# Kernel tuning notes

Measured on AMD Instinct MI355X. Metric: run time of the kernel, lower is better.

The kernel has to match this reference:

```python
import jax, jax.numpy as jnp
import numpy as np

D = 128          # embed_dim
NB = 30          # hardcoded neighbor count in neighbor_encoder
STEPS = 4        # process_steps
NSYM = 200000    # num_symbols (pad idx = NSYM)
B = 4096         # query batch
FEW = 5          # support pairs


def setup_inputs() -> dict:
    key = jax.random.key(0)
    ks = jax.random.split(key, 32)
    g = lambda i, shape, s=0.02: jax.random.normal(ks[i], shape, dtype=jnp.float32) * s
    inp = {}
    # embedding tables (row NSYM is padding, zeros)
    inp['emb'] = g(0, (NSYM + 1, D), 0.1).at[NSYM].set(0.0)
    inp['emb_var'] = g(1, (NSYM + 1, D), 0.1).at[NSYM].set(0.0)
    # neighbor attention (mean path)
    inp['nW'], inp['nWb'] = g(2, (D, 2 * D)), jnp.zeros((D,), jnp.float32)
    inp['nu'], inp['nub'] = g(3, (1, D)), jnp.zeros((1,), jnp.float32)
    # neighbor attention (var path)
    inp['nvW'], inp['nvWb'] = g(4, (D, 2 * D)), jnp.zeros((D,), jnp.float32)
    inp['nvu'], inp['nvub'] = g(5, (1, D)), jnp.zeros((1,), jnp.float32)
    # SupportEncoder: d_model=2D, d_inner=4D
    inp['p1W'], inp['p1b'] = g(6, (4 * D, 2 * D)), jnp.zeros((4 * D,), jnp.float32)
    inp['p2W'], inp['p2b'] = g(7, (2 * D, 4 * D)), jnp.zeros((2 * D,), jnp.float32)
    inp['ln_a'], inp['ln_b'] = jnp.ones((2 * D,), jnp.float32), jnp.zeros((2 * D,), jnp.float32)
    # QueryEncoder LSTMCell: input 2D, hidden 4D (torch gate order i,f,g,o)
    inp['Wih'], inp['Whh'] = g(8, (16 * D, 2 * D)), g(9, (16 * D, 4 * D))
    inp['bih'], inp['bhh'] = jnp.zeros((16 * D,), jnp.float32), jnp.zeros((16 * D,), jnp.float32)
    # connections: (..., 0)=relation idx, (..., 1)=entity idx
    inp['q_left'] = jax.random.randint(ks[10], (B, NB, 2), 0, NSYM, dtype=jnp.int32)
    inp['q_right'] = jax.random.randint(ks[11], (B, NB, 2), 0, NSYM, dtype=jnp.int32)
    inp['s_left'] = jax.random.randint(ks[12], (FEW, NB, 2), 0, NSYM, dtype=jnp.int32)
    inp['s_right'] = jax.random.randint(ks[13], (FEW, NB, 2), 0, NSYM, dtype=jnp.int32)
    return inp


def _layer_norm(z, a, b, eps=0.001):
    # faithful to torch: std with Bessel correction (ddof=1)
    mu = jnp.mean(z, axis=-1, keepdims=True)
    sigma = jnp.std(z, axis=-1, keepdims=True, ddof=1)
    return (z - mu) / (sigma + eps) * a + b


def reference(emb, emb_var, nW, nWb, nu, nub, nvW, nvWb, nvu, nvub,
              p1W, p1b, p2W, p2b, ln_a, ln_b, Wih, Whh, bih, bhh,
              q_left, q_right, s_left, s_right):

    def neighbor_encoder(conn):
        rel, ent = conn[..., 0], conn[..., 1]
        rel_e, ent_e = emb[rel], emb[ent]                      # [N, NB, D]
        cat = jnp.concatenate([rel_e, ent_e], axis=-1)         # [N, NB, 2D]
        a = jnp.tanh(cat @ nW.T + nWb) @ nu.T + nub            # [N, NB, 1]
        att = jax.nn.softmax(a[..., 0], axis=1)                # softmax over neighbors
        out = jnp.einsum('nk,nkd->nd', att, ent_e)
        rel_v, ent_v = emb_var[rel], emb_var[ent]
        catv = jnp.concatenate([rel_v, ent_v], axis=-1)
        av = jnp.tanh(catv @ nvW.T + nvWb) @ nvu.T + nvub
        attv = jax.nn.softmax(av[..., 0], axis=1)
        out_v = jnp.einsum('nk,nkd->nd', attv, ent_e)          # torch quirk: pools ent_embeds
        return jnp.tanh(out), jnp.tanh(out_v)

    def support_encoder(x):
        h = jax.nn.relu(x @ p1W.T + p1b) @ p2W.T + p2b
        return _layer_norm(h + x, ln_a, ln_b)

    def lstm_cell(x, h, c):
        gates = x @ Wih.T + bih + h @ Whh.T + bhh
        i, f, g_, o = jnp.split(gates, 4, axis=-1)
        c = jax.nn.sigmoid(f) * c + jax.nn.sigmoid(i) * jnp.tanh(g_)
        return jax.nn.sigmoid(o) * jnp.tanh(c), c

    def query_encoder(support, query):
        n = query.shape[0]
        h_r = jnp.zeros((n, 4 * D), query.dtype)
        c = jnp.zeros((n, 4 * D), query.dtype)
        h = query
        for _ in range(STEPS):
            h_r_, c = lstm_cell(query, h_r, c)
            h = query + h_r_[:, :2 * D]
            attn = jax.nn.softmax(h @ support.T, axis=1)
            r = attn @ support
            h_r = jnp.concatenate([h, r], axis=1)
        return h

    ql, qlv = neighbor_encoder(q_left)
    qr, qrv = neighbor_encoder(q_right)
    sl, slv = neighbor_encoder(s_left)
    sr, srv = neighbor_encoder(s_right)

    query = jnp.concatenate([ql, qr], axis=-1)       # [B, 2D]
    query_v = jnp.concatenate([qlv, qrv], axis=-1)
    support = jnp.concatenate([sl, sr], axis=-1)     # [FEW, 2D]
    support_v = jnp.concatenate([slv, srv], axis=-1)

    def match(q, s):
        s_g = support_encoder(s)
        q_g = support_encoder(q)
        q_f = query_encoder(s_g, q_g)
        s_mean = jnp.mean(s_g, axis=0, keepdims=True)  # [1, 2D]
        return (q_f @ s_mean.T)[:, 0]                  # [B]

    score = match(query, support)
    score_var = match(query_v, support_v)
    return jnp.stack([score, score_var])               # [2, B]
```

## Files before the change

kernel.cpp:

```cpp
#include <hip/hip_runtime.h>
#include <math.h>

#define DD    128
#define TWOD  256
#define FOURD 512
#define NBN   30
#define BQ    4096
#define FEWN  5
#define NSYM  200000
#define KTOT  768
#define NGATE 1024
#define ULIVE 256
#define TOTU  (2 * BQ + 2 * FEWN)
#define UPB   4
#define PSTR  136

typedef short bf16x8 __attribute__((ext_vector_type(8)));
typedef float f32x4 __attribute__((ext_vector_type(4)));

__device__ __forceinline__ float sigmoidf_(float x) { return 1.0f / (1.0f + expf(-x)); }

__device__ __forceinline__ float ftanh(float x) {
    float e = __expf(2.0f * x);
    return 1.0f - 2.0f / (e + 1.0f);
}

__device__ __forceinline__ unsigned short f2bf(float f) {
    unsigned int u = __float_as_uint(f);
    unsigned int r = (u + 0x7fffu + ((u >> 16) & 1u)) >> 16;
    return (unsigned short)r;
}

__device__ __forceinline__ float bf2f(unsigned short s) {
    return __uint_as_float(((unsigned int)s) << 16);
}

__device__ __forceinline__ bf16x8 pack8(float4 a, float4 b) {
    union { bf16x8 v; unsigned int u[4]; } r;
    r.u[0] = ((__float_as_uint(a.x) + 0x8000u) >> 16) | ((__float_as_uint(a.y) + 0x8000u) & 0xffff0000u);
    r.u[1] = ((__float_as_uint(a.z) + 0x8000u) >> 16) | ((__float_as_uint(a.w) + 0x8000u) & 0xffff0000u);
    r.u[2] = ((__float_as_uint(b.x) + 0x8000u) >> 16) | ((__float_as_uint(b.y) + 0x8000u) & 0xffff0000u);
    r.u[3] = ((__float_as_uint(b.z) + 0x8000u) >> 16) | ((__float_as_uint(b.w) + 0x8000u) & 0xffff0000u);
    return r.v;
}

__device__ __forceinline__ void gload_lds16(const void* g, void* l) {
    __builtin_amdgcn_global_load_lds((const __attribute__((address_space(1))) unsigned int*)g,
                                     (__attribute__((address_space(3))) unsigned int*)l,
                                     16, 0, 0);
}

__global__ __launch_bounds__(256) void k_prep(
    const float* __restrict__ Wih, const float* __restrict__ Whh,
    const float* __restrict__ bih, const float* __restrict__ bhh,
    const float* __restrict__ p1W, const float* __restrict__ p2W,
    const float* __restrict__ nW, const float* __restrict__ nvW,
    unsigned short* __restrict__ Wbf, float* __restrict__ biasR,
    float* __restrict__ p1WT, float* __restrict__ p2WT,
    unsigned short* __restrict__ Nbf)
{
    int idx = blockIdx.x * 256 + threadIdx.x;
    int stride = gridDim.x * 256;
    for (int i = idx; i < NGATE * KTOT; i += stride) {
        int n = i / KTOT, k = i - n * KTOT;
        int blk = n >> 6, rem = n & 63;
        int g = rem >> 4, ul = rem & 15;
        int u = blk * 16 + ul;
        int srcrow = g * 512 + u;
        float v = (k < TWOD) ? Wih[srcrow * TWOD + k] : Whh[srcrow * FOURD + (k - TWOD)];
        Wbf[i] = f2bf(v);
    }
    for (int n = idx; n < NGATE; n += stride) {
        int blk = n >> 6, rem = n & 63;
        int g = rem >> 4, ul = rem & 15;
        int u = blk * 16 + ul;
        int srcrow = g * 512 + u;
        biasR[n] = bih[srcrow] + bhh[srcrow];
    }
    for (int i = idx; i < FOURD * TWOD; i += stride) {
        int o = i / TWOD, j = i % TWOD;
        p1WT[j * FOURD + o] = p1W[o * TWOD + j];
    }
    for (int i = idx; i < TWOD * FOURD; i += stride) {
        int o = i / FOURD, j = i % FOURD;
        p2WT[j * TWOD + o] = p2W[o * FOURD + j];
    }
    for (int i = idx; i < 2 * DD * TWOD; i += stride) {
        float v = (i < DD * TWOD) ? nW[i] : nvW[i - DD * TWOD];
        Nbf[i] = f2bf(v);
    }
}

__global__ __launch_bounds__(256, 2) void k_neighbor_v4(
    const float* __restrict__ emb, const float* __restrict__ emb_var,
    const unsigned short* __restrict__ Nbf,
    const float* __restrict__ nWb, const float* __restrict__ nu,
    const float* __restrict__ nvWb, const float* __restrict__ nvu,
    const int* __restrict__ q_left, const int* __restrict__ q_right,
    const int* __restrict__ s_left, const int* __restrict__ s_right,
    float* __restrict__ query, float* __restrict__ support)
{
    const int tid  = threadIdx.x;
    const int wave = tid >> 6, lane = tid & 63;
    const int quad = lane >> 4, m15 = lane & 15;
    const int pw   = wave >> 1;
    const int wn   = wave & 1;
    const int u0   = blockIdx.x * UPB;

    __shared__ __align__(16) unsigned short Sg[4 * 32 * PSTR];
    __shared__ int   sidxL[UPB][64];
    __shared__ float aP[2][2][32];
    __shared__ float attL[2][32];

    {
        int un = tid >> 6, i = tid & 63;
        int uu_ = u0 + un; if (uu_ >= TOTU) uu_ = TOTU - 1;
        const int* conn;
        if (uu_ < BQ)                 conn = q_left  + uu_ * (NBN * 2);
        else if (uu_ < 2 * BQ)        conn = q_right + (uu_ - BQ) * (NBN * 2);
        else if (uu_ < 2 * BQ + FEWN) conn = s_left  + (uu_ - 2 * BQ) * (NBN * 2);
        else                          conn = s_right + (uu_ - 2 * BQ - FEWN) * (NBN * 2);
        sidxL[un][i] = (i < NBN * 2) ? conn[i] : NSYM;
    }

    const unsigned short* Bw = Nbf + (size_t)pw * DD * TWOD;
    const float* Wb = pw ? nvWb : nWb;
    const float* uu = pw ? nvu  : nu;
    bf16x8 Bf[4][8];
    float nb[4], un_[4];
#pragma unroll
    for (int t = 0; t < 4; ++t) {
        int n = wn * 64 + t * 16 + m15;
#pragma unroll
        for (int kt = 0; kt < 8; ++kt)
            Bf[t][kt] = *(const bf16x8*)(Bw + n * TWOD + kt * 32 + quad * 8);
        nb[t] = Wb[n];
        un_[t] = uu[n];
    }
    __syncthreads();

    for (int r = 0; r < UPB; ++r) {
        const int uidx = u0 + r;

        {
            const int g = wave;
            const float* table = (g < 2) ? emb : emb_var;
            const int side = g & 1;
            const int colf = (lane & 15) * 8;
            const int rsub = lane >> 4;
#pragma unroll
            for (int i = 0; i < 8; ++i) {
                int row = i * 4 + rsub;
                int sym = sidxL[r][2 * row + side];
                const float* src = table + (size_t)sym * DD + colf;
                float4 x0 = *(const float4*)src;
                float4 x1 = *(const float4*)(src + 4);
                *(bf16x8*)&Sg[(g * 32 + row) * PSTR + colf] = pack8(x0, x1);
            }
        }
        __syncthreads();

        const int pg = pw ? 2 : 0;
        f32x4 acc[2][4] = {};
#pragma unroll
        for (int kt = 0; kt < 8; ++kt) {
            const int g = (kt < 4) ? pg : pg + 1;
            const int coff = (kt & 3) * 32 + quad * 8;
            bf16x8 fa[2];
#pragma unroll
            for (int mt = 0; mt < 2; ++mt)
                fa[mt] = *(const bf16x8*)&Sg[(g * 32 + mt * 16 + m15) * PSTR + coff];
#pragma unroll
            for (int mt = 0; mt < 2; ++mt)
#pragma unroll
                for (int nt = 0; nt < 4; ++nt)
                    acc[mt][nt] = __builtin_amdgcn_mfma_f32_16x16x32_bf16(fa[mt], Bf[nt][kt], acc[mt][nt], 0, 0, 0);
        }

        {
            float part[2][4];
#pragma unroll
            for (int mt = 0; mt < 2; ++mt)
#pragma unroll
                for (int rr = 0; rr < 4; ++rr) {
                    float s = 0.f;
#pragma unroll
                    for (int nt = 0; nt < 4; ++nt)
                        s += un_[nt] * ftanh(acc[mt][nt][rr] + nb[nt]);
                    part[mt][rr] = s;
                }
#pragma unroll
            for (int off = 1; off < 16; off <<= 1)
#pragma unroll
                for (int mt = 0; mt < 2; ++mt)
#pragma unroll
                    for (int rr = 0; rr < 4; ++rr)
                        part[mt][rr] += __shfl_xor(part[mt][rr], off, 64);
            if (m15 == 0) {
#pragma unroll
                for (int mt = 0; mt < 2; ++mt)
#pragma unroll
                    for (int rr = 0; rr < 4; ++rr)
                        aP[pw][wn][mt * 16 + quad * 4 + rr] = part[mt][rr];
            }
        }
        __syncthreads();

        if ((wave & 1) == 0 && lane < 32) {
            const int p = wave >> 1;
            float sc = (lane < NBN) ? aP[p][0][lane] + aP[p][1][lane] : -1e30f;
            float mx = sc;
#pragma unroll
            for (int off = 1; off < 32; off <<= 1) mx = fmaxf(mx, __shfl_xor(mx, off, 64));
            float e = (lane < NBN) ? __expf(sc - mx) : 0.f;
            float sum = e;
#pragma unroll
            for (int off = 1; off < 32; off <<= 1) sum += __shfl_xor(sum, off, 64);
            attL[p][lane] = e / sum;
        }
        __syncthreads();

        {
            const int p = tid >> 7;
            const int d = tid & 127;
            float pool = 0.f;
#pragma unroll
            for (int k = 0; k < NBN; ++k)
                pool += attL[p][k] * bf2f(Sg[(32 + k) * PSTR + d]);
            if (uidx < TOTU) {
                float* dst;
                if (uidx < BQ)                 dst = query   + ((size_t)p * BQ + uidx) * TWOD;
                else if (uidx < 2 * BQ)        dst = query   + ((size_t)p * BQ + (uidx - BQ)) * TWOD + DD;
                else if (uidx < 2 * BQ + FEWN) dst = support + ((size_t)p * FEWN + (uidx - 2 * BQ)) * TWOD;
                else                           dst = support + ((size_t)p * FEWN + (uidx - 2 * BQ - FEWN)) * TWOD + DD;
                dst[d] = ftanh(pool);
            }
        }
        __syncthreads();
    }
}

template <int RPB>
__global__ __launch_bounds__(256) void k_supenc(
    const float* __restrict__ xin, float* __restrict__ xout,
    unsigned short* __restrict__ abf,
    const float* __restrict__ p1WT, const float* __restrict__ p1b,
    const float* __restrict__ p2WT, const float* __restrict__ p2b,
    const float* __restrict__ ln_a, const float* __restrict__ ln_b)
{
    const int tid = threadIdx.x;
    const int r0 = blockIdx.x * RPB;
    __shared__ float X[RPB][TWOD];
    __shared__ float H1[RPB][FOURD];
    __shared__ float red[4][RPB][2];
    __shared__ float muv[RPB], sgv[RPB];

    for (int idx = tid; idx < RPB * TWOD; idx += 256) {
        int r = idx >> 8, j = idx & 255;
        X[r][j] = xin[(size_t)(r0 + r) * TWOD + j];
    }
    __syncthreads();

    {
        float acc[RPB][2] = {};
        for (int j = 0; j < TWOD; j += 4) {
            float w0[4], w1[4];
#pragma unroll
            for (int jj = 0; jj < 4; ++jj) {
                w0[jj] = p1WT[(j + jj) * FOURD + tid];
                w1[jj] = p1WT[(j + jj) * FOURD + tid + 256];
            }
#pragma unroll
            for (int r = 0; r < RPB; ++r) {
                float x[4] __attribute__((aligned(16)));
                *(float4*)x = *(const float4*)&X[r][j];
#pragma unroll
                for (int jj = 0; jj < 4; ++jj) {
                    acc[r][0] += x[jj] * w0[jj];
                    acc[r][1] += x[jj] * w1[jj];
                }
            }
        }
        float b0 = p1b[tid], b1 = p1b[tid + 256];
#pragma unroll
        for (int r = 0; r < RPB; ++r) {
            H1[r][tid]       = fmaxf(acc[r][0] + b0, 0.f);
            H1[r][tid + 256] = fmaxf(acc[r][1] + b1, 0.f);
        }
    }
    __syncthreads();

    float z[RPB];
    {
        float acc[RPB] = {};
        for (int j = 0; j < FOURD; j += 4) {
            float w[4];
#pragma unroll
            for (int jj = 0; jj < 4; ++jj) w[jj] = p2WT[(j + jj) * TWOD + tid];
#pragma unroll
            for (int r = 0; r < RPB; ++r) {
                float h[4] __attribute__((aligned(16)));
                *(float4*)h = *(const float4*)&H1[r][j];
#pragma unroll
                for (int jj = 0; jj < 4; ++jj) acc[r] += h[jj] * w[jj];
            }
        }
        float b = p2b[tid];
#pragma unroll
        for (int r = 0; r < RPB; ++r) z[r] = acc[r] + b + X[r][tid];
    }
    {
        float s[RPB], ss[RPB];
#pragma unroll
        for (int r = 0; r < RPB; ++r) { s[r] = z[r]; ss[r] = z[r] * z[r]; }
#pragma unroll
        for (int off = 1; off < 64; off <<= 1)
#pragma unroll
            for (int r = 0; r < RPB; ++r) {
                s[r]  += __shfl_xor(s[r],  off, 64);
                ss[r] += __shfl_xor(ss[r], off, 64);
            }
        const int wv = tid >> 6, lane = tid & 63;
        if (lane == 0) {
#pragma unroll
            for (int r = 0; r < RPB; ++r) { red[wv][r][0] = s[r]; red[wv][r][1] = ss[r]; }
        }
        __syncthreads();
        if (tid < RPB) {
            float st  = red[0][tid][0] + red[1][tid][0] + red[2][tid][0] + red[3][tid][0];
            float sst = red[0][tid][1] + red[1][tid][1] + red[2][tid][1] + red[3][tid][1];
            float mu  = st / (float)TWOD;
            float var = fmaxf((sst - (float)TWOD * mu * mu) / ((float)TWOD - 1.f), 0.f);
            muv[tid] = mu; sgv[tid] = sqrtf(var);
        }
        __syncthreads();
    }
#pragma unroll
    for (int r = 0; r < RPB; ++r) {
        float o = (z[r] - muv[r]) / (sgv[r] + 1e-3f) * ln_a[tid] + ln_b[tid];
        xout[(size_t)(r0 + r) * TWOD + tid] = o;
        if (abf) abf[(size_t)(r0 + r) * KTOT + tid] = f2bf(o);
    }
}

__global__ __launch_bounds__(256) void k_lstm_mfma(
    const unsigned short* __restrict__ Abf,
    const unsigned short* __restrict__ Wbf,
    const float* __restrict__ biasR,
    float* __restrict__ cst, float* __restrict__ hbuf,
    const int nkt)
{
    __shared__ __align__(16) unsigned short As[2 * 2 * 4096];
    __shared__ __align__(16) unsigned short Bs[2 * 2 * 4096];
    const int tid  = threadIdx.x;
    const int wave = tid >> 6, lane = tid & 63;
    const int quad = lane >> 4, m15 = lane & 15;
    const int m0 = blockIdx.x * 128;
    const int n0 = blockIdx.y * 128;
    const int wm = wave >> 1, wn = wave & 1;
    const int lrow = lane >> 2, lslot = lane & 3;

    f32x4 acc[4][4] = {};

    auto stage = [&](int buf, int k0) {
#pragma unroll
        for (int t = 0; t < 2; ++t) {
            const int c = wave * 2 + t;
            const int row = c * 16 + lrow;
            const int kg = lslot ^ ((row >> 1) & 3);
#pragma unroll
            for (int kh = 0; kh < 2; ++kh) {
                gload_lds16(Abf + (size_t)(m0 + row) * KTOT + k0 + kh * 32 + kg * 8,
                            As + buf * 8192 + kh * 4096 + c * 512);
                gload_lds16(Wbf + (size_t)(n0 + row) * KTOT + k0 + kh * 32 + kg * 8,
                            Bs + buf * 8192 + kh * 4096 + c * 512);
            }
        }
    };

    auto compute = [&](int buf) {
#pragma unroll
        for (int kh = 0; kh < 2; ++kh) {
            const unsigned short* pA = As + buf * 8192 + kh * 4096;
            const unsigned short* pB = Bs + buf * 8192 + kh * 4096;
            bf16x8 fa[4], fb[4];
#pragma unroll
            for (int mi = 0; mi < 4; ++mi) {
                int ra = wm * 64 + mi * 16 + m15;
                int sa = quad ^ ((ra >> 1) & 3);
                fa[mi] = *(const bf16x8*)(pA + ra * 32 + sa * 8);
                int rb = wn * 64 + mi * 16 + m15;
                int sb = quad ^ ((rb >> 1) & 3);
                fb[mi] = *(const bf16x8*)(pB + rb * 32 + sb * 8);
            }
#pragma unroll
            for (int mi = 0; mi < 4; ++mi)
#pragma unroll
                for (int ni = 0; ni < 4; ++ni)
                    acc[mi][ni] = __builtin_amdgcn_mfma_f32_16x16x32_bf16(fa[mi], fb[ni], acc[mi][ni], 0, 0, 0);
        }
    };

    stage(0, 0);
    __syncthreads();

    int cur = 0;
    for (int kt = 0; kt < nkt; ++kt) {
        if (kt + 1 < nkt) stage(cur ^ 1, (kt + 1) * 64);
        compute(cur);
        __syncthreads();
        cur ^= 1;
    }

    const int u = ((n0 + wn * 64) >> 2) + m15;
    float bg[4];
#pragma unroll
    for (int g = 0; g < 4; ++g) bg[g] = biasR[n0 + wn * 64 + g * 16 + m15];
#pragma unroll
    for (int mi = 0; mi < 4; ++mi) {
#pragma unroll
        for (int r = 0; r < 4; ++r) {
            int gm = m0 + wm * 64 + mi * 16 + quad * 4 + r;
            size_t cidx = (size_t)gm * ULIVE + u;
            float pi = acc[mi][0][r] + bg[0];
            float pf = acc[mi][1][r] + bg[1];
            float pg = acc[mi][2][r] + bg[2];
            float po = acc[mi][3][r] + bg[3];
            float cn = sigmoidf_(pf) * cst[cidx] + sigmoidf_(pi) * tanhf(pg);
            cst[cidx]  = cn;
            hbuf[cidx] = sigmoidf_(po) * tanhf(cn);
        }
    }
}

__global__ __launch_bounds__(256) void k_lstm_attn(
    const float* __restrict__ qg, const float* __restrict__ hbuf,
    const float* __restrict__ sg, unsigned short* __restrict__ Abf,
    float* __restrict__ hfin)
{
    const int tid = threadIdx.x;
    const int p   = blockIdx.y;
    const int wv = tid >> 6, lane = tid & 63;
    __shared__ float sgl[FEWN][TWOD];
    for (int idx = tid; idx < FEWN * TWOD; idx += 256)
        sgl[idx >> 8][idx & 255] = sg[p * FEWN * TWOD + idx];
    __syncthreads();
    const int j0 = lane * 4;
    for (int rr = 0; rr < 8; ++rr) {
        int row = blockIdx.x * 32 + wv * 8 + rr;
        size_t g = (size_t)p * BQ + row;
        float4 q4 = *(const float4*)(qg + g * TWOD + j0);
        float4 t4 = *(const float4*)(hbuf + g * ULIVE + j0);
        float h[4] __attribute__((aligned(16))) = {q4.x + t4.x, q4.y + t4.y, q4.z + t4.z, q4.w + t4.w};
        float sv[FEWN][4] __attribute__((aligned(16)));
        float pa[FEWN];
#pragma unroll
        for (int f = 0; f < FEWN; ++f) {
            *(float4*)sv[f] = *(const float4*)&sgl[f][j0];
            pa[f] = h[0] * sv[f][0] + h[1] * sv[f][1] + h[2] * sv[f][2] + h[3] * sv[f][3];
        }
#pragma unroll
        for (int off = 1; off < 64; off <<= 1)
#pragma unroll
            for (int f = 0; f < FEWN; ++f) pa[f] += __shfl_xor(pa[f], off, 64);
        float mx = pa[0];
#pragma unroll
        for (int f = 1; f < FEWN; ++f) mx = fmaxf(mx, pa[f]);
        float sum = 0.f, e[FEWN];
#pragma unroll
        for (int f = 0; f < FEWN; ++f) { e[f] = expf(pa[f] - mx); sum += e[f]; }
        float inv = 1.f / sum;
        float r4[4] __attribute__((aligned(16))) = {0.f, 0.f, 0.f, 0.f};
#pragma unroll
        for (int f = 0; f < FEWN; ++f) {
            float a = e[f] * inv;
#pragma unroll
            for (int q = 0; q < 4; ++q) r4[q] += a * sv[f][q];
        }
        unsigned short tb[4] __attribute__((aligned(8)));
#pragma unroll
        for (int q = 0; q < 4; ++q) tb[q] = f2bf(h[q]);
        *(uint2*)(Abf + g * KTOT + TWOD + j0) = *(uint2*)tb;
#pragma unroll
        for (int q = 0; q < 4; ++q) tb[q] = f2bf(r4[q]);
        *(uint2*)(Abf + g * KTOT + FOURD + j0) = *(uint2*)tb;
        *(float4*)(hfin + g * TWOD + j0) = *(float4*)h;
    }
}

__global__ __launch_bounds__(256) void k_score(
    const float* __restrict__ hfin, const float* __restrict__ sg, float* __restrict__ out)
{
    const int tid = threadIdx.x;
    const int p   = blockIdx.y;
    __shared__ float sm[TWOD];
    if (tid < TWOD) {
        const float* s = sg + p * FEWN * TWOD + tid;
        sm[tid] = (s[0] + s[TWOD] + s[2 * TWOD] + s[3 * TWOD] + s[4 * TWOD]) / 5.0f;
    }
    __syncthreads();
    const int wv = tid >> 6, lane = tid & 63;
    const int j0 = lane * 4;
    for (int rr = 0; rr < 8; ++rr) {
        int row = blockIdx.x * 32 + wv * 8 + rr;
        const float* h = hfin + ((size_t)p * BQ + row) * TWOD + j0;
        float4 h4 = *(const float4*)h;
        float4 s4 = *(const float4*)&sm[j0];
        float pv = h4.x * s4.x + h4.y * s4.y + h4.z * s4.z + h4.w * s4.w;
#pragma unroll
        for (int off = 1; off < 64; off <<= 1) pv += __shfl_xor(pv, off, 64);
        if (lane == 0) out[p * BQ + row] = pv;
    }
}

extern "C" void kernel_launch(void* const* d_in, const int* in_sizes, int n_in,
                              void* d_out, int out_size, void* d_ws, size_t ws_size,
                              hipStream_t stream)
{
    const float* emb     = (const float*)d_in[0];
    const float* emb_var = (const float*)d_in[1];
    const float* nW      = (const float*)d_in[2];
    const float* nWb     = (const float*)d_in[3];
    const float* nu      = (const float*)d_in[4];
    const float* nub     = (const float*)d_in[5];
    const float* nvW     = (const float*)d_in[6];
    const float* nvWb    = (const float*)d_in[7];
    const float* nvu     = (const float*)d_in[8];
    const float* nvub    = (const float*)d_in[9];
    const float* p1W     = (const float*)d_in[10];
    const float* p1b     = (const float*)d_in[11];
    const float* p2W     = (const float*)d_in[12];
    const float* p2b     = (const float*)d_in[13];
    const float* ln_a    = (const float*)d_in[14];
    const float* ln_b    = (const float*)d_in[15];
    const float* Wih     = (const float*)d_in[16];
    const float* Whh     = (const float*)d_in[17];
    const float* bih     = (const float*)d_in[18];
    const float* bhh     = (const float*)d_in[19];
    const int* q_left    = (const int*)d_in[20];
    const int* q_right   = (const int*)d_in[21];
    const int* s_left    = (const int*)d_in[22];
    const int* s_right   = (const int*)d_in[23];

    float* ws = (float*)d_ws;
    size_t o = 0;
    float* p1WT     = ws + o; o += FOURD * TWOD;
    float* p2WT     = ws + o; o += FOURD * TWOD;
    float* biasR    = ws + o; o += NGATE;
    float* query    = ws + o; o += (size_t)2 * BQ * TWOD;
    float* supportB = ws + o; o += 2 * FEWN * TWOD;
    float* qg       = ws + o; o += (size_t)2 * BQ * TWOD;
    float* sg       = ws + o; o += 2 * FEWN * TWOD;
    float* cst      = ws + o; o += (size_t)2 * BQ * ULIVE;
    float* hbuf     = ws + o; o += (size_t)2 * BQ * ULIVE;
    unsigned short* Wbf = (unsigned short*)(ws + o); o += (size_t)NGATE * KTOT / 2;
    unsigned short* Abf = (unsigned short*)(ws + o); o += (size_t)2 * BQ * KTOT / 2;
    unsigned short* Nbf = (unsigned short*)(ws + o); o += (size_t)2 * DD * TWOD / 2;
    float* hfin     = query;

    hipMemsetAsync(cst, 0, (size_t)2 * BQ * ULIVE * sizeof(float), stream);

    k_prep<<<dim3(1024), dim3(256), 0, stream>>>(Wih, Whh, bih, bhh, p1W, p2W, nW, nvW,
                                                 Wbf, biasR, p1WT, p2WT, Nbf);
    k_neighbor_v4<<<dim3((TOTU + UPB - 1) / UPB), dim3(256), 0, stream>>>(
        emb, emb_var, Nbf, nWb, nu, nvWb, nvu,
        q_left, q_right, s_left, s_right, query, supportB);
    k_supenc<8><<<dim3(2 * BQ / 8), dim3(256), 0, stream>>>(query, qg, Abf, p1WT, p1b, p2WT, p2b, ln_a, ln_b);
    k_supenc<1><<<dim3(2 * FEWN), dim3(256), 0, stream>>>(supportB, sg, (unsigned short*)nullptr,
                                                          p1WT, p1b, p2WT, p2b, ln_a, ln_b);
    for (int s = 0; s < 4; ++s) {
        k_lstm_mfma<<<dim3(2 * BQ / 128, NGATE / 128), dim3(256), 0, stream>>>(
            Abf, Wbf, biasR, cst, hbuf, s == 0 ? TWOD / 64 : KTOT / 64);
        k_lstm_attn<<<dim3(BQ / 32, 2), dim3(256), 0, stream>>>(qg, hbuf, sg, Abf, hfin);
    }
    k_score<<<dim3(BQ / 32, 2), dim3(256), 0, stream>>>(hfin, sg, (float*)d_out);
}
```

Measured before the change: 590.0 us.

## Store LSTM hidden state in bf16, fuse scoring into last attention step

```diff
diff --git a/kernel.cpp b/kernel.cpp
--- a/kernel.cpp
+++ b/kernel.cpp
@@ -338,8 +338,8 @@
 #pragma unroll
     for (int r = 0; r < RPB; ++r) {
         float o = (z[r] - muv[r]) / (sgv[r] + 1e-3f) * ln_a[tid] + ln_b[tid];
-        xout[(size_t)(r0 + r) * TWOD + tid] = o;
-        if (abf) abf[(size_t)(r0 + r) * KTOT + tid] = f2bf(o);
+        if (xout) xout[(size_t)(r0 + r) * TWOD + tid] = o;
+        if (abf)  abf[(size_t)(r0 + r) * KTOT + tid] = f2bf(o);
     }
 }
 
@@ -347,8 +347,8 @@
     const unsigned short* __restrict__ Abf,
     const unsigned short* __restrict__ Wbf,
     const float* __restrict__ biasR,
-    float* __restrict__ cst, float* __restrict__ hbuf,
-    const int nkt)
+    float* __restrict__ cst, unsigned short* __restrict__ hbufB,
+    const int nkt, const int first)
 {
     __shared__ __align__(16) unsigned short As[2 * 2 * 4096];
     __shared__ __align__(16) unsigned short Bs[2 * 2 * 4096];
@@ -426,32 +426,43 @@
             float pf = acc[mi][1][r] + bg[1];
             float pg = acc[mi][2][r] + bg[2];
             float po = acc[mi][3][r] + bg[3];
-            float cn = sigmoidf_(pf) * cst[cidx] + sigmoidf_(pi) * tanhf(pg);
-            cst[cidx]  = cn;
-            hbuf[cidx] = sigmoidf_(po) * tanhf(cn);
+            float cprev = 0.f;
+            if (!first) cprev = cst[cidx];
+            float cn = sigmoidf_(pf) * cprev + sigmoidf_(pi) * tanhf(pg);
+            cst[cidx]   = cn;
+            hbufB[cidx] = f2bf(sigmoidf_(po) * tanhf(cn));
         }
     }
 }
 
 __global__ __launch_bounds__(256) void k_lstm_attn(
-    const float* __restrict__ qg, const float* __restrict__ hbuf,
+    const unsigned short* __restrict__ hbufB,
     const float* __restrict__ sg, unsigned short* __restrict__ Abf,
-    float* __restrict__ hfin)
+    float* __restrict__ out, const int final_)
 {
     const int tid = threadIdx.x;
     const int p   = blockIdx.y;
     const int wv = tid >> 6, lane = tid & 63;
     __shared__ float sgl[FEWN][TWOD];
+    __shared__ float sm[TWOD];
     for (int idx = tid; idx < FEWN * TWOD; idx += 256)
         sgl[idx >> 8][idx & 255] = sg[p * FEWN * TWOD + idx];
     __syncthreads();
+    if (final_) {
+        if (tid < TWOD)
+            sm[tid] = (sgl[0][tid] + sgl[1][tid] + sgl[2][tid] + sgl[3][tid] + sgl[4][tid]) * 0.2f;
+        __syncthreads();
+    }
     const int j0 = lane * 4;
     for (int rr = 0; rr < 8; ++rr) {
         int row = blockIdx.x * 32 + wv * 8 + rr;
         size_t g = (size_t)p * BQ + row;
-        float4 q4 = *(const float4*)(qg + g * TWOD + j0);
-        float4 t4 = *(const float4*)(hbuf + g * ULIVE + j0);
-        float h[4] __attribute__((aligned(16))) = {q4.x + t4.x, q4.y + t4.y, q4.z + t4.z, q4.w + t4.w};
+        union { uint2 v; unsigned short s[4]; } qq, tt;
+        qq.v = *(const uint2*)(Abf + g * KTOT + j0);
+        tt.v = *(const uint2*)(hbufB + g * ULIVE + j0);
+        float h[4] __attribute__((aligned(16)));
+#pragma unroll
+        for (int q = 0; q < 4; ++q) h[q] = bf2f(qq.s[q]) + bf2f(tt.s[q]);
         float sv[FEWN][4] __attribute__((aligned(16)));
         float pa[FEWN];
 #pragma unroll
@@ -463,53 +474,35 @@
         for (int off = 1; off < 64; off <<= 1)
 #pragma unroll
             for (int f = 0; f < FEWN; ++f) pa[f] += __shfl_xor(pa[f], off, 64);
-        float mx = pa[0];
-#pragma unroll
-        for (int f = 1; f < FEWN; ++f) mx = fmaxf(mx, pa[f]);
-        float sum = 0.f, e[FEWN];
-#pragma unroll
-        for (int f = 0; f < FEWN; ++f) { e[f] = expf(pa[f] - mx); sum += e[f]; }
-        float inv = 1.f / sum;
-        float r4[4] __attribute__((aligned(16))) = {0.f, 0.f, 0.f, 0.f};
-#pragma unroll
-        for (int f = 0; f < FEWN; ++f) {
-            float a = e[f] * inv;
-#pragma unroll
-            for (int q = 0; q < 4; ++q) r4[q] += a * sv[f][q];
-        }
-        unsigned short tb[4] __attribute__((aligned(8)));
-#pragma unroll
-        for (int q = 0; q < 4; ++q) tb[q] = f2bf(h[q]);
-        *(uint2*)(Abf + g * KTOT + TWOD + j0) = *(uint2*)tb;
-#pragma unroll
-        for (int q = 0; q < 4; ++q) tb[q] = f2bf(r4[q]);
-        *(uint2*)(Abf + g * KTOT + FOURD + j0) = *(uint2*)tb;
-        *(float4*)(hfin + g * TWOD + j0) = *(float4*)h;
-    }
-}
-
-__global__ __launch_bounds__(256) void k_score(
-    const float* __restrict__ hfin, const float* __restrict__ sg, float* __restrict__ out)
-{
-    const int tid = threadIdx.x;
-    const int p   = blockIdx.y;
-    __shared__ float sm[TWOD];
-    if (tid < TWOD) {
-        const float* s = sg + p * FEWN * TWOD + tid;
-        sm[tid] = (s[0] + s[TWOD] + s[2 * TWOD] + s[3 * TWOD] + s[4 * TWOD]) / 5.0f;
-    }
-    __syncthreads();
-    const int wv = tid >> 6, lane = tid & 63;
-    const int j0 = lane * 4;
-    for (int rr = 0; rr < 8; ++rr) {
-        int row = blockIdx.x * 32 + wv * 8 + rr;
-        const float* h = hfin + ((size_t)p * BQ + row) * TWOD + j0;
-        float4 h4 = *(const float4*)h;
-        float4 s4 = *(const float4*)&sm[j0];
-        float pv = h4.x * s4.x + h4.y * s4.y + h4.z * s4.z + h4.w * s4.w;
-#pragma unroll
-        for (int off = 1; off < 64; off <<= 1) pv += __shfl_xor(pv, off, 64);
-        if (lane == 0) out[p * BQ + row] = pv;
+        if (!final_) {
+            float mx = pa[0];
+#pragma unroll
+            for (int f = 1; f < FEWN; ++f) mx = fmaxf(mx, pa[f]);
+            float sum = 0.f, e[FEWN];
+#pragma unroll
+            for (int f = 0; f < FEWN; ++f) { e[f] = expf(pa[f] - mx); sum += e[f]; }
+            float inv = 1.f / sum;
+            float r4[4] __attribute__((aligned(16))) = {0.f, 0.f, 0.f, 0.f};
+#pragma unroll
+            for (int f = 0; f < FEWN; ++f) {
+                float a = e[f] * inv;
+#pragma unroll
+                for (int q = 0; q < 4; ++q) r4[q] += a * sv[f][q];
+            }
+            unsigned short tb[4] __attribute__((aligned(8)));
+#pragma unroll
+            for (int q = 0; q < 4; ++q) tb[q] = f2bf(h[q]);
+            *(uint2*)(Abf + g * KTOT + TWOD + j0) = *(uint2*)tb;
+#pragma unroll
+            for (int q = 0; q < 4; ++q) tb[q] = f2bf(r4[q]);
+            *(uint2*)(Abf + g * KTOT + FOURD + j0) = *(uint2*)tb;
+        } else {
+            const float* s4 = &sm[j0];
+            float pv = h[0] * s4[0] + h[1] * s4[1] + h[2] * s4[2] + h[3] * s4[3];
+#pragma unroll
+            for (int off = 1; off < 64; off <<= 1) pv += __shfl_xor(pv, off, 64);
+            if (lane == 0) out[p * BQ + row] = pv;
+        }
     }
 }
 
@@ -549,29 +542,27 @@
     float* biasR    = ws + o; o += NGATE;
     float* query    = ws + o; o += (size_t)2 * BQ * TWOD;
     float* supportB = ws + o; o += 2 * FEWN * TWOD;
-    float* qg       = ws + o; o += (size_t)2 * BQ * TWOD;
     float* sg       = ws + o; o += 2 * FEWN * TWOD;
     float* cst      = ws + o; o += (size_t)2 * BQ * ULIVE;
-    float* hbuf     = ws + o; o += (size_t)2 * BQ * ULIVE;
-    unsigned short* Wbf = (unsigned short*)(ws + o); o += (size_t)NGATE * KTOT / 2;
-    unsigned short* Abf = (unsigned short*)(ws + o); o += (size_t)2 * BQ * KTOT / 2;
-    unsigned short* Nbf = (unsigned short*)(ws + o); o += (size_t)2 * DD * TWOD / 2;
-    float* hfin     = query;
-
-    hipMemsetAsync(cst, 0, (size_t)2 * BQ * ULIVE * sizeof(float), stream);
+    unsigned short* hbufB = (unsigned short*)(ws + o); o += (size_t)2 * BQ * ULIVE / 2;
+    unsigned short* Wbf   = (unsigned short*)(ws + o); o += (size_t)NGATE * KTOT / 2;
+    unsigned short* Abf   = (unsigned short*)(ws + o); o += (size_t)2 * BQ * KTOT / 2;
+    unsigned short* Nbf   = (unsigned short*)(ws + o); o += (size_t)2 * DD * TWOD / 2;
+
 
     k_prep<<<dim3(1024), dim3(256), 0, stream>>>(Wih, Whh, bih, bhh, p1W, p2W, nW, nvW,
                                                  Wbf, biasR, p1WT, p2WT, Nbf);
     k_neighbor_v4<<<dim3((TOTU + UPB - 1) / UPB), dim3(256), 0, stream>>>(
         emb, emb_var, Nbf, nWb, nu, nvWb, nvu,
         q_left, q_right, s_left, s_right, query, supportB);
-    k_supenc<8><<<dim3(2 * BQ / 8), dim3(256), 0, stream>>>(query, qg, Abf, p1WT, p1b, p2WT, p2b, ln_a, ln_b);
+    k_supenc<8><<<dim3(2 * BQ / 8), dim3(256), 0, stream>>>(query, (float*)nullptr, Abf,
+                                                            p1WT, p1b, p2WT, p2b, ln_a, ln_b);
     k_supenc<1><<<dim3(2 * FEWN), dim3(256), 0, stream>>>(supportB, sg, (unsigned short*)nullptr,
                                                           p1WT, p1b, p2WT, p2b, ln_a, ln_b);
     for (int s = 0; s < 4; ++s) {
         k_lstm_mfma<<<dim3(2 * BQ / 128, NGATE / 128), dim3(256), 0, stream>>>(
-            Abf, Wbf, biasR, cst, hbuf, s == 0 ? TWOD / 64 : KTOT / 64);
-        k_lstm_attn<<<dim3(BQ / 32, 2), dim3(256), 0, stream>>>(qg, hbuf, sg, Abf, hfin);
-    }
-    k_score<<<dim3(BQ / 32, 2), dim3(256), 0, stream>>>(hfin, sg, (float*)d_out);
-}
+            Abf, Wbf, biasR, cst, hbufB, s == 0 ? TWOD / 64 : KTOT / 64, s == 0 ? 1 : 0);
+        k_lstm_attn<<<dim3(BQ / 32, 2), dim3(256), 0, stream>>>(
+            hbufB, sg, Abf, (float*)d_out, s == 3 ? 1 : 0);
+    }
+}
```

Result: no change. 583.9 us (-1.0%).
